# Performance work log

Measured on AMD Instinct MI355X. Metric: run time of the kernel, lower is better.

## Reference

```python
import jax, jax.numpy as jnp
import numpy as np

B, S, D, H = 4, 2048, 1024, 16
DH = D // H


def setup_inputs() -> dict:
    key = jax.random.key(0)
    k1, k2, k3, k4, k5 = jax.random.split(key, 5)
    X = jax.random.normal(k1, (B, S, D), dtype=jnp.float32)
    W1 = jax.random.normal(k2, (3 * D, D), dtype=jnp.float32) * 0.02
    b1 = jax.random.normal(k3, (3 * D,), dtype=jnp.float32) * 0.01
    W2 = jax.random.normal(k4, (D, D), dtype=jnp.float32) * 0.02
    b2 = jax.random.normal(k5, (D,), dtype=jnp.float32) * 0.01
    return {"X": X, "W1": W1, "b1": b1, "W2": W2, "b2": b2}


def reference(X, W1, b1, W2, b2):
    b, s, d = X.shape
    # fused QKV projection (nn.Linear: y = x @ W.T + b)
    Y = X @ W1.T + b1                                   # [B,S,3D]
    Q, K, V = jnp.split(Y, 3, axis=2)                   # each [B,S,D]
    # reshape(x): view (B,S,H,DH) then permute(0,2,3,1) -> [B,H,DH,S]
    q = Q.reshape(b, s, H, DH).transpose(0, 2, 3, 1)    # [B,H,DH,S]
    v = V.reshape(b, s, H, DH).transpose(0, 2, 3, 1)    # [B,H,DH,S]
    # reshape(x, k=True): permute(0,2,1,3) -> [B,H,S,DH]
    k = K.reshape(b, s, H, DH).transpose(0, 2, 1, 3)    # [B,H,S,DH]
    # w = q @ k / sqrt(q.size(-1)) ; note q.size(-1) == S in this layout
    w = jnp.einsum('bhds,bhse->bhde', q, k) / jnp.sqrt(jnp.asarray(s, X.dtype))  # [B,H,DH,DH]
    w = jax.nn.softmax(w, axis=-1)
    out = jnp.einsum('bhde,bhes->bhds', w, v)           # [B,H,DH,S]
    # cat(): raw contiguous view of [B,H,DH,S] into [B,S,H*DH] (memory-order reshape)
    out = out.reshape(b, s, H * DH)                     # [B,S,D]
    return out @ W2.T + b2
```

## Files before the change

kernel.cpp:

```cpp
#include <hip/hip_runtime.h>
#include <stdint.h>

#define B_ 4
#define S_ 2048
#define D_ 1024
#define H_ 16
#define DH_ 64
#define M_TOT (B_*S_)
#define N1_ (3*D_)
#define K_ D_
#define NCH 8

typedef __bf16 bf16_8 __attribute__((ext_vector_type(8)));
typedef float  f32x4  __attribute__((ext_vector_type(4)));

typedef __attribute__((address_space(1))) const void* gas_t;
typedef __attribute__((address_space(3))) void*       las_t;

__device__ __forceinline__ unsigned short f2bf(float f) {
    union { float f; unsigned u; } v; v.f = f;
    unsigned r = v.u + 0x7FFFu + ((v.u >> 16) & 1u);
    return (unsigned short)(r >> 16);
}

__device__ __forceinline__ void async_ld16(const void* g, void* l) {
    __builtin_amdgcn_global_load_lds((gas_t)g, (las_t)l, 16, 0, 0);
}

__global__ __launch_bounds__(256)
void cast_kernel(const float* __restrict__ X, const float* __restrict__ W1,
                 const float* __restrict__ W2, unsigned short* __restrict__ Xb,
                 unsigned short* __restrict__ W1b, unsigned short* __restrict__ W2b) {
    const int nX  = (M_TOT * K_) / 4;
    const int nW1 = (N1_ * K_) / 4;
    int i = blockIdx.x * 256 + threadIdx.x;
    const float4* src; unsigned short* dst; int j;
    if (i < nX)            { src = (const float4*)X;  dst = Xb;  j = i; }
    else if (i < nX + nW1) { src = (const float4*)W1; dst = W1b; j = i - nX; }
    else                   { src = (const float4*)W2; dst = W2b; j = i - nX - nW1; }
    float4 v = src[j];
    ushort4 o;
    o.x = f2bf(v.x); o.y = f2bf(v.y); o.z = f2bf(v.z); o.w = f2bf(v.w);
    ((ushort4*)dst)[j] = o;
}

template<int N, int NBX, bool OUT_BF16>
__global__ __launch_bounds__(256)
void gemm_bt(const unsigned short* __restrict__ A,
             const unsigned short* __restrict__ Bm,
             const float* __restrict__ bias,
             void* __restrict__ C, int K) {
    __shared__ unsigned short As[128 * 64];
    __shared__ unsigned short Bs[128 * 64];
    const int t    = threadIdx.x;
    const int wid  = t >> 6;
    const int lane = t & 63;
    const int lrow = lane & 15;
    const int lq   = lane >> 4;

    const int lid  = blockIdx.y * NBX + blockIdx.x;
    const int xcd  = lid & 7;
    const int slot = lid >> 3;
    const int by   = xcd * (gridDim.y >> 3) + slot / NBX;
    const int bx   = slot % NBX;
    const int m0   = by * 128;
    const int n0   = bx * 128;

    const int wm   = (wid >> 1) * 64;
    const int wn   = (wid & 1) * 64;

    f32x4 acc[4][4] = {};

    for (int k0 = 0; k0 < K; k0 += 64) {
#pragma unroll
        for (int p = 0; p < 4; p++) {
            const int c   = p * 256 + t;
            const int row = c >> 3;
            const int kb  = (c & 7) ^ (row & 7);
            async_ld16(A  + (size_t)(m0 + row) * K + k0 + kb * 8, (char*)As + c * 16);
            async_ld16(Bm + (size_t)(n0 + row) * K + k0 + kb * 8, (char*)Bs + c * 16);
        }
        __syncthreads();

#pragma unroll
        for (int ks = 0; ks < 2; ks++) {
            bf16_8 af[4], bfr[4];
#pragma unroll
            for (int mt = 0; mt < 4; mt++) {
                const int r  = wm + mt * 16 + lrow;
                const int kb = (ks * 4 + lq) ^ (r & 7);
                af[mt] = *(const bf16_8*)(As + (r * 8 + kb) * 8);
            }
#pragma unroll
            for (int nt = 0; nt < 4; nt++) {
                const int r  = wn + nt * 16 + lrow;
                const int kb = (ks * 4 + lq) ^ (r & 7);
                bfr[nt] = *(const bf16_8*)(Bs + (r * 8 + kb) * 8);
            }
#pragma unroll
            for (int mt = 0; mt < 4; mt++)
#pragma unroll
                for (int nt = 0; nt < 4; nt++)
                    acc[mt][nt] = __builtin_amdgcn_mfma_f32_16x16x32_bf16(af[mt], bfr[nt], acc[mt][nt], 0, 0, 0);
        }
        __syncthreads();
    }

#pragma unroll
    for (int nt = 0; nt < 4; nt++) {
        const int col = n0 + wn + nt * 16 + lrow;
        const float bv = bias[col];
#pragma unroll
        for (int mt = 0; mt < 4; mt++) {
            const int row = m0 + wm + mt * 16 + lq * 4;
            f32x4 a = acc[mt][nt];
            if (OUT_BF16) {
                unsigned short* Cp = (unsigned short*)C;
#pragma unroll
                for (int i = 0; i < 4; i++)
                    Cp[(size_t)(row + i) * N + col] = f2bf(a[i] + bv);
            } else {
                float* Cp = (float*)C;
#pragma unroll
                for (int i = 0; i < 4; i++)
                    Cp[(size_t)(row + i) * N + col] = a[i] + bv;
            }
        }
    }
}

__global__ __launch_bounds__(256)
void attn_scores(const unsigned short* __restrict__ Y, float* __restrict__ Scp) {
    __shared__ unsigned short Qs[64 * 72];
    __shared__ unsigned short Ks[64 * 72];
    const int bh = blockIdx.x, ch = blockIdx.y;
    const int b = bh >> 4, h = bh & 15;
    const size_t ybase = (size_t)b * S_ * 3072;
    const int qoff = h * 64, koff = D_ + h * 64;
    const int t = threadIdx.x, wid = t >> 6, lane = t & 63;
    const int lrow = lane & 15, lq = lane >> 4;

    f32x4 acc[4] = {};
    const int sbeg = ch * (S_ / NCH);
    for (int s0 = sbeg; s0 < sbeg + S_ / NCH; s0 += 64) {
#pragma unroll
        for (int p = 0; p < 4; p++) {
            int idx = p * 256 + t;
            int r = idx >> 4, cg = (idx & 15) * 4;
            const size_t gb = ybase + (size_t)(s0 + r) * 3072;
            ushort4 q4 = *(const ushort4*)(Y + gb + qoff + cg);
            ushort4 k4 = *(const ushort4*)(Y + gb + koff + cg);
            Qs[(cg + 0) * 72 + r] = q4.x; Qs[(cg + 1) * 72 + r] = q4.y;
            Qs[(cg + 2) * 72 + r] = q4.z; Qs[(cg + 3) * 72 + r] = q4.w;
            Ks[(cg + 0) * 72 + r] = k4.x; Ks[(cg + 1) * 72 + r] = k4.y;
            Ks[(cg + 2) * 72 + r] = k4.z; Ks[(cg + 3) * 72 + r] = k4.w;
        }
        __syncthreads();
#pragma unroll
        for (int ks = 0; ks < 2; ks++) {
            bf16_8 aq = *(const bf16_8*)(Qs + (wid * 16 + lrow) * 72 + ks * 32 + lq * 8);
#pragma unroll
            for (int nt = 0; nt < 4; nt++) {
                bf16_8 bk = *(const bf16_8*)(Ks + (nt * 16 + lrow) * 72 + ks * 32 + lq * 8);
                acc[nt] = __builtin_amdgcn_mfma_f32_16x16x32_bf16(aq, bk, acc[nt], 0, 0, 0);
            }
        }
        __syncthreads();
    }

    float* out = Scp + (size_t)(bh * NCH + ch) * 64 * 64;
#pragma unroll
    for (int nt = 0; nt < 4; nt++)
#pragma unroll
        for (int i = 0; i < 4; i++)
            out[(wid * 16 + lq * 4 + i) * 64 + nt * 16 + lrow] = acc[nt][i];
}

__global__ __launch_bounds__(256)
void attn_softmax(const float* __restrict__ Scp, unsigned short* __restrict__ Wb) {
    const int bh = blockIdx.x;
    const int t = threadIdx.x;
    const int d = t >> 2, q = t & 3;
    float s[16] = {};
#pragma unroll
    for (int c = 0; c < NCH; c++) {
        const float4* p = (const float4*)(Scp + ((size_t)(bh * NCH + c) * 64 + d) * 64 + q * 16);
#pragma unroll
        for (int j = 0; j < 4; j++) {
            float4 v = p[j];
            s[j*4+0] += v.x; s[j*4+1] += v.y; s[j*4+2] += v.z; s[j*4+3] += v.w;
        }
    }
    const float scale = 0.022097086912079608f;
    float m = -3.0e38f;
#pragma unroll
    for (int i = 0; i < 16; i++) { s[i] *= scale; m = fmaxf(m, s[i]); }
    m = fmaxf(m, __shfl_xor(m, 1));
    m = fmaxf(m, __shfl_xor(m, 2));
    float sum = 0.f;
#pragma unroll
    for (int i = 0; i < 16; i++) { s[i] = __expf(s[i] - m); sum += s[i]; }
    sum += __shfl_xor(sum, 1);
    sum += __shfl_xor(sum, 2);
    const float inv = 1.0f / sum;
    unsigned short* w = Wb + (size_t)bh * 4096 + d * 64 + q * 16;
    ushort4 o0, o1, o2, o3;
    o0.x=f2bf(s[0]*inv);  o0.y=f2bf(s[1]*inv);  o0.z=f2bf(s[2]*inv);  o0.w=f2bf(s[3]*inv);
    o1.x=f2bf(s[4]*inv);  o1.y=f2bf(s[5]*inv);  o1.z=f2bf(s[6]*inv);  o1.w=f2bf(s[7]*inv);
    o2.x=f2bf(s[8]*inv);  o2.y=f2bf(s[9]*inv);  o2.z=f2bf(s[10]*inv); o2.w=f2bf(s[11]*inv);
    o3.x=f2bf(s[12]*inv); o3.y=f2bf(s[13]*inv); o3.z=f2bf(s[14]*inv); o3.w=f2bf(s[15]*inv);
    ((ushort4*)w)[0]=o0; ((ushort4*)w)[1]=o1; ((ushort4*)w)[2]=o2; ((ushort4*)w)[3]=o3;
}

__global__ __launch_bounds__(256)
void attn_out(const unsigned short* __restrict__ Y, const unsigned short* __restrict__ Wb,
              unsigned short* __restrict__ O) {
    __shared__ unsigned short Ws[64 * 72];
    const int bh = blockIdx.x, sc = blockIdx.y;
    const int b = bh >> 4, h = bh & 15;
    const size_t ybase = (size_t)b * S_ * 3072;
    const int voff = 2 * D_ + h * 64;
    const int t = threadIdx.x, wid = t >> 6, lane = t & 63;
    const int lrow = lane & 15, lq = lane >> 4;

    {
        const int d = t >> 2, q = t & 3;
        const uint4* src = (const uint4*)(Wb + (size_t)bh * 4096 + d * 64 + q * 16);
        uint4* dst = (uint4*)(Ws + d * 72 + q * 16);
        dst[0] = src[0];
        *(uint4*)(Ws + d * 72 + q * 16 + 8) = src[1];
    }
    __syncthreads();

    bf16_8 aw[4][2];
#pragma unroll
    for (int mt = 0; mt < 4; mt++)
#pragma unroll
        for (int ks = 0; ks < 2; ks++)
            aw[mt][ks] = *(const bf16_8*)(Ws + (mt * 16 + lrow) * 72 + ks * 32 + lq * 8);

    const size_t obase = (size_t)b * (H_ * DH_ * S_) + (size_t)h * (DH_ * S_);
    const int s0 = sc * 256 + wid * 64;
    f32x4 o[4][4] = {};
#pragma unroll
    for (int ks = 0; ks < 2; ks++) {
        bf16_8 bv[4];
#pragma unroll
        for (int nt = 0; nt < 4; nt++)
            bv[nt] = *(const bf16_8*)(Y + ybase + (size_t)(s0 + nt * 16 + lrow) * 3072 + voff + ks * 32 + lq * 8);
#pragma unroll
        for (int mt = 0; mt < 4; mt++)
#pragma unroll
            for (int nt = 0; nt < 4; nt++)
                o[mt][nt] = __builtin_amdgcn_mfma_f32_16x16x32_bf16(aw[mt][ks], bv[nt], o[mt][nt], 0, 0, 0);
    }
#pragma unroll
    for (int mt = 0; mt < 4; mt++)
#pragma unroll
        for (int nt = 0; nt < 4; nt++) {
            const int d = mt * 16 + lq * 4;
            const int s = s0 + nt * 16 + lrow;
#pragma unroll
            for (int i = 0; i < 4; i++)
                O[obase + (size_t)(d + i) * S_ + s] = f2bf(o[mt][nt][i]);
        }
}

extern "C" void kernel_launch(void* const* d_in, const int* in_sizes, int n_in,
                              void* d_out, int out_size, void* d_ws, size_t ws_size,
                              hipStream_t stream) {
    const float* X  = (const float*)d_in[0];
    const float* W1 = (const float*)d_in[1];
    const float* b1 = (const float*)d_in[2];
    const float* W2 = (const float*)d_in[3];
    const float* b2 = (const float*)d_in[4];

    char* ws = (char*)d_ws;
    unsigned short* Xb  = (unsigned short*)(ws + 0);
    unsigned short* W1b = (unsigned short*)(ws + (16u << 20));
    unsigned short* W2b = (unsigned short*)(ws + (22u << 20));
    unsigned short* Yb  = (unsigned short*)(ws + (24u << 20));
    unsigned short* Wb  = (unsigned short*)(ws + 0);
    unsigned short* Ob  = (unsigned short*)(ws + (1u << 20));
    float* Scp = (float*)d_out;

    cast_kernel<<<12288, 256, 0, stream>>>(X, W1, W2, Xb, W1b, W2b);
    gemm_bt<N1_, N1_/128, true><<<dim3(N1_ / 128, M_TOT / 128), 256, 0, stream>>>(Xb, W1b, b1, Yb, K_);
    attn_scores<<<dim3(64, NCH), 256, 0, stream>>>(Yb, Scp);
    attn_softmax<<<64, 256, 0, stream>>>(Scp, Wb);
    attn_out<<<dim3(64, NCH), 256, 0, stream>>>(Yb, Wb, Ob);
    gemm_bt<D_, D_/128, false><<<dim3(D_ / 128, M_TOT / 128), 256, 0, stream>>>(Ob, W2b, b2, d_out, K_);
}
```

Measured before the change: 213.0 us.

## Replace GEMM with 256x256-tile double-buffered 8-wave pipelined kernel

Replaces the 128x128 single-buffered bf16 GEMM with a 256x256-tile, 512-thread kernel. It double-buffers A/B tiles in LDS and interleaves async global-to-LDS loads with quarter-tile MFMA blocks under explicit barriers, vmcnt waits and setprio hints. The aim is to hide global load latency behind MFMA work and raise arithmetic intensity per tile. The cost is 128KB of LDS per block and far fewer blocks, with 128 blocks for the output projection, which risks lower occupancy and poor CU fill on the smaller GEMM.

```diff
diff --git a/kernel.cpp b/kernel.cpp
--- a/kernel.cpp
+++ b/kernel.cpp
@@ -13,6 +13,7 @@
 
 typedef __bf16 bf16_8 __attribute__((ext_vector_type(8)));
 typedef float  f32x4  __attribute__((ext_vector_type(4)));
+typedef unsigned short u16;
 
 typedef __attribute__((address_space(1))) const void* gas_t;
 typedef __attribute__((address_space(3))) void*       las_t;
@@ -44,86 +45,160 @@
     ((ushort4*)dst)[j] = o;
 }
 
-template<int N, int NBX, bool OUT_BF16>
-__global__ __launch_bounds__(256)
-void gemm_bt(const unsigned short* __restrict__ A,
-             const unsigned short* __restrict__ Bm,
-             const float* __restrict__ bias,
-             void* __restrict__ C, int K) {
-    __shared__ unsigned short As[128 * 64];
-    __shared__ unsigned short Bs[128 * 64];
+
+#define LDA_H(AS, MH, AF) do {                                                     \
+  _Pragma("unroll") for (int m_ = 0; m_ < 4; m_++)                                 \
+  _Pragma("unroll") for (int ks_ = 0; ks_ < 2; ks_++) {                            \
+    const int rho_ = (MH)*128 + wr*64 + m_*16 + lrow;                              \
+    AF[m_][ks_] = *(const bf16_8*)((const u16*)(AS) + rho_*64 +                    \
+                                   (((ks_*4+lq) ^ (lrow&7)) << 3)); } } while (0)
+
+#define LDB_H(BS, NH, BF) do {                                                     \
+  _Pragma("unroll") for (int n_ = 0; n_ < 2; n_++)                                 \
+  _Pragma("unroll") for (int ks_ = 0; ks_ < 2; ks_++) {                            \
+    const int rho_ = (NH)*128 + wc*32 + n_*16 + lrow;                              \
+    BF[n_][ks_] = *(const bf16_8*)((const u16*)(BS) + rho_*64 +                    \
+                                   (((ks_*4+lq) ^ (lrow&7)) << 3)); } } while (0)
+
+#define MMA_Q(MH, NH, AF, BF) do {                                                 \
+    __builtin_amdgcn_s_setprio(1);                                                 \
+    _Pragma("unroll") for (int ks_ = 0; ks_ < 2; ks_++)                            \
+    _Pragma("unroll") for (int m_ = 0; m_ < 4; m_++)                               \
+    _Pragma("unroll") for (int n_ = 0; n_ < 2; n_++)                               \
+        acc[(MH)*4+m_][(NH)*2+n_] = __builtin_amdgcn_mfma_f32_16x16x32_bf16(       \
+            AF[m_][ks_], BF[n_][ks_], acc[(MH)*4+m_][(NH)*2+n_], 0, 0, 0);         \
+    __builtin_amdgcn_s_setprio(0);                                                 \
+  } while (0)
+
+#define BAR()      __builtin_amdgcn_s_barrier()
+#define WAIT_LGKM() asm volatile("s_waitcnt lgkmcnt(0)" ::: "memory")
+
+template<int N, int NBX, int KK, bool OUT_BF16>
+__global__ __launch_bounds__(512, 2)
+void gemm_bt2(const u16* __restrict__ A, const u16* __restrict__ Bm,
+              const float* __restrict__ bias, void* __restrict__ C) {
+    __shared__ u16 As[2][256 * 64];
+    __shared__ u16 Bs[2][256 * 64];
+
     const int t    = threadIdx.x;
     const int wid  = t >> 6;
     const int lane = t & 63;
     const int lrow = lane & 15;
     const int lq   = lane >> 4;
+    const int wr   = wid >> 2;
+    const int wc   = wid & 3;
 
     const int lid  = blockIdx.y * NBX + blockIdx.x;
     const int xcd  = lid & 7;
     const int slot = lid >> 3;
     const int by   = xcd * (gridDim.y >> 3) + slot / NBX;
     const int bx   = slot % NBX;
-    const int m0   = by * 128;
-    const int n0   = bx * 128;
-
-    const int wm   = (wid >> 1) * 64;
-    const int wn   = (wid & 1) * 64;
-
-    f32x4 acc[4][4] = {};
-
-    for (int k0 = 0; k0 < K; k0 += 64) {
-#pragma unroll
-        for (int p = 0; p < 4; p++) {
-            const int c   = p * 256 + t;
-            const int row = c >> 3;
-            const int kb  = (c & 7) ^ (row & 7);
-            async_ld16(A  + (size_t)(m0 + row) * K + k0 + kb * 8, (char*)As + c * 16);
-            async_ld16(Bm + (size_t)(n0 + row) * K + k0 + kb * 8, (char*)Bs + c * 16);
-        }
-        __syncthreads();
-
-#pragma unroll
-        for (int ks = 0; ks < 2; ks++) {
-            bf16_8 af[4], bfr[4];
-#pragma unroll
-            for (int mt = 0; mt < 4; mt++) {
-                const int r  = wm + mt * 16 + lrow;
-                const int kb = (ks * 4 + lq) ^ (r & 7);
-                af[mt] = *(const bf16_8*)(As + (r * 8 + kb) * 8);
-            }
-#pragma unroll
-            for (int nt = 0; nt < 4; nt++) {
-                const int r  = wn + nt * 16 + lrow;
-                const int kb = (ks * 4 + lq) ^ (r & 7);
-                bfr[nt] = *(const bf16_8*)(Bs + (r * 8 + kb) * 8);
-            }
-#pragma unroll
-            for (int mt = 0; mt < 4; mt++)
-#pragma unroll
-                for (int nt = 0; nt < 4; nt++)
-                    acc[mt][nt] = __builtin_amdgcn_mfma_f32_16x16x32_bf16(af[mt], bfr[nt], acc[mt][nt], 0, 0, 0);
-        }
-        __syncthreads();
+    const int m0   = by * 256;
+    const int n0   = bx * 256;
+
+    const u16* Ab = A  + (size_t)m0 * KK;
+    const u16* Bb = Bm + (size_t)n0 * KK;
+
+    f32x4 acc[8][4] = {};
+
+    auto STG = [&](const u16* __restrict__ G, char* lds, int half, int k0, bool isA) {
+#pragma unroll
+        for (int cc = 0; cc < 2; cc++) {
+            const int rho = half * 128 + cc * 64 + (t >> 3);
+            const int blk = t & 7;
+            const int g   = isA ? (((rho >> 6) & 1) * 128 + ((rho >> 7) & 1) * 64 + (rho & 63))
+                                : (((rho >> 5) & 3) * 64  + ((rho >> 7) & 1) * 32 + (rho & 31));
+            async_ld16(G + (size_t)g * KK + k0 + ((blk ^ (rho & 7)) << 3),
+                       lds + rho * 128 + blk * 16);
+        }
+    };
+
+    char* as0 = (char*)&As[0][0]; char* as1 = (char*)&As[1][0];
+    char* bs0 = (char*)&Bs[0][0]; char* bs1 = (char*)&Bs[1][0];
+
+    STG(Ab, as0, 0, 0,  true);
+    STG(Bb, bs0, 0, 0,  false);
+    STG(Bb, bs0, 1, 0,  false);
+    STG(Ab, as0, 1, 0,  true);
+    STG(Ab, as1, 0, 64, true);
+    STG(Bb, bs1, 0, 64, false);
+    STG(Bb, bs1, 1, 64, false);
+    asm volatile("s_waitcnt vmcnt(6)" ::: "memory");
+    BAR();
+
+    bf16_8 af[4][2], blo[2][2], bhi[2][2];
+
+    constexpr int NT = KK / 64;
+    constexpr int NI = NT / 2;
+
+    for (int i = 0; i < NI; ++i) {
+        const bool pf = (i < NI - 1);
+        const int kE = (2 * i + 2) * 64;
+        const int kO = (2 * i + 3) * 64;
+
+        LDA_H(as0, 0, af);
+        LDB_H(bs0, 0, blo);
+        STG(Ab, as1, 1, (2 * i + 1) * 64, true);
+        BAR(); WAIT_LGKM();
+        MMA_Q(0, 0, af, blo);
+        BAR();
+        LDB_H(bs0, 1, bhi);
+        if (pf) STG(Ab, as0, 0, kE, true);
+        BAR(); WAIT_LGKM();
+        MMA_Q(0, 1, af, bhi);
+        BAR();
+        LDA_H(as0, 1, af);
+        if (pf) STG(Bb, bs0, 0, kE, false);
+        BAR(); WAIT_LGKM();
+        MMA_Q(1, 1, af, bhi);
+        BAR();
+        if (pf) STG(Bb, bs0, 1, kE, false);
+        BAR();
+        MMA_Q(1, 0, af, blo);
+        if (pf) { asm volatile("s_waitcnt vmcnt(6)" ::: "memory"); }
+        else    { asm volatile("s_waitcnt vmcnt(0)" ::: "memory"); }
+        BAR();
+        LDA_H(as1, 0, af);
+        LDB_H(bs1, 0, blo);
+        if (pf) STG(Ab, as0, 1, kE, true);
+        BAR(); WAIT_LGKM();
+        MMA_Q(0, 0, af, blo);
+        BAR();
+        LDB_H(bs1, 1, bhi);
+        if (pf) STG(Ab, as1, 0, kO, true);
+        BAR(); WAIT_LGKM();
+        MMA_Q(0, 1, af, bhi);
+        BAR();
+        LDA_H(as1, 1, af);
+        if (pf) STG(Bb, bs1, 0, kO, false);
+        BAR(); WAIT_LGKM();
+        MMA_Q(1, 1, af, bhi);
+        BAR();
+        if (pf) STG(Bb, bs1, 1, kO, false);
+        BAR();
+        MMA_Q(1, 0, af, blo);
+        if (pf) asm volatile("s_waitcnt vmcnt(6)" ::: "memory");
+        BAR();
     }
 
 #pragma unroll
     for (int nt = 0; nt < 4; nt++) {
-        const int col = n0 + wn + nt * 16 + lrow;
+        const int col = n0 + wc * 64 + nt * 16 + lrow;
         const float bv = bias[col];
 #pragma unroll
-        for (int mt = 0; mt < 4; mt++) {
-            const int row = m0 + wm + mt * 16 + lq * 4;
+        for (int mt = 0; mt < 8; mt++) {
+            const int row = m0 + wr * 128 + mt * 16 + lq * 4;
             f32x4 a = acc[mt][nt];
             if (OUT_BF16) {
-                unsigned short* Cp = (unsigned short*)C;
-#pragma unroll
-                for (int i = 0; i < 4; i++)
-                    Cp[(size_t)(row + i) * N + col] = f2bf(a[i] + bv);
+                u16* Cp = (u16*)C;
+#pragma unroll
+                for (int i2 = 0; i2 < 4; i2++)
+                    Cp[(size_t)(row + i2) * N + col] = f2bf(a[i2] + bv);
             } else {
                 float* Cp = (float*)C;
 #pragma unroll
-                for (int i = 0; i < 4; i++)
-                    Cp[(size_t)(row + i) * N + col] = a[i] + bv;
+                for (int i2 = 0; i2 < 4; i2++)
+                    Cp[(size_t)(row + i2) * N + col] = a[i2] + bv;
             }
         }
     }
@@ -285,9 +360,9 @@
     float* Scp = (float*)d_out;
 
     cast_kernel<<<12288, 256, 0, stream>>>(X, W1, W2, Xb, W1b, W2b);
-    gemm_bt<N1_, N1_/128, true><<<dim3(N1_ / 128, M_TOT / 128), 256, 0, stream>>>(Xb, W1b, b1, Yb, K_);
+    gemm_bt2<N1_, N1_/256, K_, true ><<<dim3(N1_ / 256, M_TOT / 256), 512, 0, stream>>>(Xb, W1b, b1, Yb);
     attn_scores<<<dim3(64, NCH), 256, 0, stream>>>(Yb, Scp);
     attn_softmax<<<64, 256, 0, stream>>>(Scp, Wb);
     attn_out<<<dim3(64, NCH), 256, 0, stream>>>(Yb, Wb, Ob);
-    gemm_bt<D_, D_/128, false><<<dim3(D_ / 128, M_TOT / 128), 256, 0, stream>>>(Ob, W2b, b2, d_out, K_);
-}
+    gemm_bt2<D_, D_/256, K_, false><<<dim3(D_ / 256, M_TOT / 256), 512, 0, stream>>>(Ob, W2b, b2, d_out);
+}
```

Measured after the change: 230.3 us. +8.1%, slower.
